# Performance work log

Measured on AMD Instinct MI355X. Metric: run time of the kernel, lower is better.

## Reference

```python
import jax, jax.numpy as jnp
import numpy as np

DIM = 1024
H = 16
HD = DIM // H
HIDDEN = 4096
EPS = 1e-5


def layer_norm(x, w, b):
    mu = jnp.mean(x, axis=-1, keepdims=True)
    var = jnp.mean(jnp.square(x - mu), axis=-1, keepdims=True)
    return (x - mu) * jax.lax.rsqrt(var + EPS) * w + b


def setup_inputs() -> dict:
    key = jax.random.key(0)
    ks = jax.random.split(key, 12)
    B, N = 4, 1024
    s = 0.02
    return {
        "x": jax.random.normal(ks[0], (B, N, DIM), jnp.float32),
        "rel_pos_bias": jax.random.normal(ks[1], (H, N, N), jnp.float32) * 0.1,
        "attn_mask": jax.random.randint(ks[2], (B, N), 0, 2, jnp.int32),
        "norm1_w": jnp.ones((DIM,), jnp.float32),
        "norm1_b": jnp.zeros((DIM,), jnp.float32),
        "qkv_w": jax.random.normal(ks[3], (3 * DIM, DIM), jnp.float32) * s,
        "q_bias": jnp.zeros((DIM,), jnp.float32),
        "v_bias": jnp.zeros((DIM,), jnp.float32),
        "proj_w": jax.random.normal(ks[4], (DIM, DIM), jnp.float32) * s,
        "proj_b": jnp.zeros((DIM,), jnp.float32),
        "norm2_w": jnp.ones((DIM,), jnp.float32),
        "norm2_b": jnp.zeros((DIM,), jnp.float32),
        "mlp_w1": jax.random.normal(ks[5], (HIDDEN, DIM), jnp.float32) * s,
        "mlp_b1": jnp.zeros((HIDDEN,), jnp.float32),
        "mlp_w2": jax.random.normal(ks[6], (DIM, HIDDEN), jnp.float32) * s,
        "mlp_b2": jnp.zeros((DIM,), jnp.float32),
    }


def attention(x, rel_pos_bias, attn_mask, qkv_w, q_bias, v_bias, proj_w, proj_b):
    B, N, C = x.shape
    scale = HD ** (-0.5)
    qkv_bias = jnp.concatenate([q_bias, jnp.zeros_like(v_bias), v_bias])
    qkv = x @ qkv_w.T + qkv_bias  # [B,N,3C]
    qkv = qkv.reshape(B, N, 3, H, HD).transpose(2, 0, 3, 1, 4)  # [3,B,H,N,hd]
    q, k, v = qkv[0] * scale, qkv[1], qkv[2]
    attn = jnp.einsum("bhqd,bhkd->bhqk", q, k) + rel_pos_bias[None]
    mask = attn_mask.astype(bool)[:, None, None, :]  # key padding mask
    attn = jnp.where(mask, attn, -jnp.inf)
    attn = jax.nn.softmax(attn, axis=-1)
    out = jnp.einsum("bhqk,bhkd->bhqd", attn, v)
    out = out.transpose(0, 2, 1, 3).reshape(B, N, C)
    return out @ proj_w.T + proj_b


def mlp(x, w1, b1, w2, b2):
    h = jax.nn.gelu(x @ w1.T + b1, approximate=False)
    return h @ w2.T + b2


def reference(x, rel_pos_bias, attn_mask, norm1_w, norm1_b, qkv_w, q_bias, v_bias,
              proj_w, proj_b, norm2_w, norm2_b, mlp_w1, mlp_b1, mlp_w2, mlp_b2):
    # pre-norm block, gamma=None, postnorm=False
    x = x + attention(layer_norm(x, norm1_w, norm1_b), rel_pos_bias, attn_mask,
                      qkv_w, q_bias, v_bias, proj_w, proj_b)
    x = x + mlp(layer_norm(x, norm2_w, norm2_b), mlp_w1, mlp_b1, mlp_w2, mlp_b2)
    return x
```

## Files before the change

### kernel.cpp

```cpp
#include <hip/hip_runtime.h>
#include <math.h>

#define DIM 1024
#define NHEAD 16
#define HD 64
#define HIDDEN 4096
#define SEQ 1024
#define BATCH 4
#define ROWS (BATCH*SEQ)

typedef __attribute__((ext_vector_type(8))) short bf16x8;
typedef __attribute__((ext_vector_type(4))) float f32x4;
typedef __attribute__((ext_vector_type(4))) unsigned short us4;

__device__ __forceinline__ unsigned short f2bf(float f) {
  unsigned u = __builtin_bit_cast(unsigned, f);
  u += 0x7fffu + ((u >> 16) & 1u);
  return (unsigned short)(u >> 16);
}

__device__ __forceinline__ float bf2f(unsigned short h) {
  unsigned u = (unsigned)h << 16;
  return __builtin_bit_cast(float, u);
}

__device__ __forceinline__ unsigned pkbf(float a, float b) {
  unsigned ua = __builtin_bit_cast(unsigned, a) + 0x8000u;
  unsigned ub = __builtin_bit_cast(unsigned, b) + 0x8000u;
  return __builtin_amdgcn_perm(ub, ua, 0x07060302u);
}

__device__ __forceinline__ float f3(float a, float b, float c) {
  return fmaxf(fmaxf(a, b), c);
}

__device__ __forceinline__ void glds16(const void* g, void* l) {
  __builtin_amdgcn_global_load_lds((const __attribute__((address_space(1))) void*)g,
                                   (__attribute__((address_space(3))) void*)l,
                                   16, 0, 0);
}

__global__ void cvt_all(const float* __restrict__ a, const float* __restrict__ b,
                        const float* __restrict__ c, const float* __restrict__ d,
                        unsigned short* __restrict__ oa, unsigned short* __restrict__ ob,
                        unsigned short* __restrict__ oc, unsigned short* __restrict__ od) {
  const int na = 3 * DIM * DIM / 4, nb = DIM * DIM / 4, nc = HIDDEN * DIM / 4, nd = DIM * HIDDEN / 4;
  const int total = na + nb + nc + nd;
  for (int i = blockIdx.x * blockDim.x + threadIdx.x; i < total; i += gridDim.x * blockDim.x) {
    const float* in; unsigned short* out; int j = i;
    if (j < na)             { in = a; out = oa; }
    else if ((j -= na) < nb){ in = b; out = ob; }
    else if ((j -= nb) < nc){ in = c; out = oc; }
    else                    { j -= nc; in = d; out = od; }
    float4 v = reinterpret_cast<const float4*>(in)[j];
    us4 o = { f2bf(v.x), f2bf(v.y), f2bf(v.z), f2bf(v.w) };
    reinterpret_cast<us4*>(out)[j] = o;
  }
}

template<bool IN_BF16>
__global__ void ln_kernel(const void* __restrict__ xv, const float* __restrict__ w,
                          const float* __restrict__ b, unsigned short* __restrict__ out) {
  int row = blockIdx.x;
  int t = threadIdx.x;
  float4 v;
  if (IN_BF16) {
    const unsigned short* xr = (const unsigned short*)xv + (size_t)row * DIM;
    us4 hv = *reinterpret_cast<const us4*>(xr + t * 4);
    v.x = bf2f(hv[0]); v.y = bf2f(hv[1]); v.z = bf2f(hv[2]); v.w = bf2f(hv[3]);
  } else {
    const float* xr = (const float*)xv + (size_t)row * DIM;
    v = *reinterpret_cast<const float4*>(xr + t * 4);
  }
  float s  = v.x + v.y + v.z + v.w;
  float s2 = v.x*v.x + v.y*v.y + v.z*v.z + v.w*v.w;
#pragma unroll
  for (int m = 1; m < 64; m <<= 1) { s += __shfl_xor(s, m); s2 += __shfl_xor(s2, m); }
  __shared__ float red[8];
  int wv = t >> 6, ln = t & 63;
  if (ln == 0) { red[wv] = s; red[4 + wv] = s2; }
  __syncthreads();
  s  = red[0] + red[1] + red[2] + red[3];
  s2 = red[4] + red[5] + red[6] + red[7];
  float mu  = s * (1.0f / DIM);
  float var = s2 * (1.0f / DIM) - mu * mu;
  float rs  = rsqrtf(var + 1e-5f);
  float4 wv4 = *reinterpret_cast<const float4*>(w + t * 4);
  float4 bv4 = *reinterpret_cast<const float4*>(b + t * 4);
  us4 o = { f2bf((v.x - mu) * rs * wv4.x + bv4.x),
            f2bf((v.y - mu) * rs * wv4.y + bv4.y),
            f2bf((v.z - mu) * rs * wv4.z + bv4.z),
            f2bf((v.w - mu) * rs * wv4.w + bv4.w) };
  *reinterpret_cast<us4*>(out + (size_t)row * DIM + t * 4) = o;
}

template<int MODE>
__global__ __launch_bounds__(256)
void gemm128k(const unsigned short* __restrict__ A, const unsigned short* __restrict__ Bw,
              int K, int N,
              const float* __restrict__ bias,
              unsigned short* __restrict__ outh)
{
  __shared__ unsigned short smA[2][128 * 64];
  __shared__ unsigned short smB[2][128 * 64];
  const int tid = threadIdx.x;
  const int wv = tid >> 6, ln = tid & 63;
  const int tile_m = blockIdx.x * 128, tile_n = blockIdx.y * 128;
  const int wm = (wv >> 1) * 64, wn = (wv & 1) * 64;

  const int srow8 = ln >> 3;
  const int sch8  = (ln & 7) ^ srow8;
  const unsigned short* gA = A  + (size_t)(tile_m + wv * 8 + srow8) * K + sch8 * 8;
  const unsigned short* gB = Bw + (size_t)(tile_n + wv * 8 + srow8) * K + sch8 * 8;

  f32x4 acc[4][4] = {};
  const int lr = ln & 15, g = ln >> 4;
  const int rx = lr & 7;

  auto stage = [&](int buf, int k0) {
#pragma unroll
    for (int p = 0; p < 4; p++)
      glds16(gA + (size_t)(p * 32) * K + k0, &smA[buf][(p * 32 + wv * 8) * 64]);
#pragma unroll
    for (int p = 0; p < 4; p++)
      glds16(gB + (size_t)(p * 32) * K + k0, &smB[buf][(p * 32 + wv * 8) * 64]);
  };

  stage(0, 0);
  __syncthreads();
  int cur = 0;
  for (int k0 = 0; k0 < K; k0 += 64) {
    if (k0 + 64 < K) stage(cur ^ 1, k0 + 64);
    bf16x8 af[4][2], bfr[4][2];
#pragma unroll
    for (int i = 0; i < 4; i++)
#pragma unroll
      for (int c = 0; c < 2; c++)
        af[i][c] = *reinterpret_cast<const bf16x8*>(
            &smA[cur][(wm + i * 16 + lr) * 64 + ((c * 4 + g) ^ rx) * 8]);
#pragma unroll
    for (int j = 0; j < 4; j++)
#pragma unroll
      for (int c = 0; c < 2; c++)
        bfr[j][c] = *reinterpret_cast<const bf16x8*>(
            &smB[cur][(wn + j * 16 + lr) * 64 + ((c * 4 + g) ^ rx) * 8]);
#pragma unroll
    for (int c = 0; c < 2; c++)
#pragma unroll
      for (int i = 0; i < 4; i++)
#pragma unroll
        for (int j = 0; j < 4; j++)
          acc[i][j] = __builtin_amdgcn_mfma_f32_16x16x32_bf16(af[i][c], bfr[j][c], acc[i][j], 0, 0, 0);
    __syncthreads();
    cur ^= 1;
  }

  const int lcol = ln & 15, lrow4 = (ln >> 4) * 4;
#pragma unroll
  for (int i = 0; i < 4; i++) {
#pragma unroll
    for (int j = 0; j < 4; j++) {
      int gm0 = tile_m + wm + i * 16 + lrow4;
      int gn  = tile_n + wn + j * 16 + lcol;
#pragma unroll
      for (int r = 0; r < 4; r++) {
        int gm = gm0 + r;
        float t2 = acc[i][j][r] + bias[gn];
        float u2 = 1.5957691216f * (t2 + 0.044715f * t2 * t2 * t2);
        float e  = __expf(u2);
        float th = 1.0f - 2.0f / (e + 1.0f);
        float gl = 0.5f * t2 * (1.0f + th);
        outh[(size_t)gm * N + gn] = f2bf(gl);
      }
    }
  }
}

template<int MODE>
__global__ __launch_bounds__(256)
void gemm64k(const unsigned short* __restrict__ A, const unsigned short* __restrict__ Bw,
             int K, int N,
             const float* __restrict__ bias, const void* __restrict__ resid,
             float* __restrict__ outf, unsigned short* __restrict__ outh,
             unsigned short* __restrict__ qo, unsigned short* __restrict__ ko,
             unsigned short* __restrict__ vto,
             const float* __restrict__ qbias, const float* __restrict__ vbias)
{
  __shared__ unsigned short smA[2][128 * 64];
  __shared__ unsigned short smB[2][64 * 64];
  const int tid = threadIdx.x;
  const int wv = tid >> 6, ln = tid & 63;
  const int tile_m = blockIdx.x * 128, tile_n = blockIdx.y * 64;
  const int wm = (wv >> 1) * 64, wn = (wv & 1) * 32;

  const int srow8 = ln >> 3;
  const int sch8  = (ln & 7) ^ srow8;
  const unsigned short* gA = A  + (size_t)(tile_m + wv * 8 + srow8) * K + sch8 * 8;
  const unsigned short* gB = Bw + (size_t)(tile_n + wv * 8 + srow8) * K + sch8 * 8;

  f32x4 acc[4][2] = {};
  const int lr = ln & 15, g = ln >> 4;
  const int rx = lr & 7;

  auto stage = [&](int buf, int k0) {
#pragma unroll
    for (int p = 0; p < 4; p++)
      glds16(gA + (size_t)(p * 32) * K + k0, &smA[buf][(p * 32 + wv * 8) * 64]);
#pragma unroll
    for (int p = 0; p < 2; p++)
      glds16(gB + (size_t)(p * 32) * K + k0, &smB[buf][(p * 32 + wv * 8) * 64]);
  };

  stage(0, 0);
  __syncthreads();
  int cur = 0;
  for (int k0 = 0; k0 < K; k0 += 64) {
    if (k0 + 64 < K) stage(cur ^ 1, k0 + 64);
    bf16x8 af[4][2], bfr[2][2];
#pragma unroll
    for (int i = 0; i < 4; i++)
#pragma unroll
      for (int c = 0; c < 2; c++)
        af[i][c] = *reinterpret_cast<const bf16x8*>(
            &smA[cur][(wm + i * 16 + lr) * 64 + ((c * 4 + g) ^ rx) * 8]);
#pragma unroll
    for (int j = 0; j < 2; j++)
#pragma unroll
      for (int c = 0; c < 2; c++)
        bfr[j][c] = *reinterpret_cast<const bf16x8*>(
            &smB[cur][(wn + j * 16 + lr) * 64 + ((c * 4 + g) ^ rx) * 8]);
#pragma unroll
    for (int c = 0; c < 2; c++)
#pragma unroll
      for (int i = 0; i < 4; i++)
#pragma unroll
        for (int j = 0; j < 2; j++)
          acc[i][j] = __builtin_amdgcn_mfma_f32_16x16x32_bf16(af[i][c], bfr[j][c], acc[i][j], 0, 0, 0);
    __syncthreads();
    cur ^= 1;
  }

  const int lcol = ln & 15, lrow4 = (ln >> 4) * 4;
#pragma unroll
  for (int i = 0; i < 4; i++) {
#pragma unroll
    for (int j = 0; j < 2; j++) {
      int gm0 = tile_m + wm + i * 16 + lrow4;
      int gn  = tile_n + wn + j * 16 + lcol;
#pragma unroll
      for (int r = 0; r < 4; r++) {
        int gm = gm0 + r;
        float val = acc[i][j][r];
        if (MODE == 0) {
          int b = gm >> 10, n = gm & 1023;
          if (gn < DIM) {
            float q = (val + qbias[gn]) * 0.125f;
            qo[(size_t)((b * NHEAD + (gn >> 6)) * SEQ + n) * HD + (gn & 63)] = f2bf(q);
          } else if (gn < 2 * DIM) {
            int g2 = gn - DIM;
            ko[(size_t)((b * NHEAD + (g2 >> 6)) * SEQ + n) * HD + (g2 & 63)] = f2bf(val);
          } else {
            int g3 = gn - 2 * DIM;
            vto[(size_t)((b * NHEAD + (g3 >> 6)) * HD + (g3 & 63)) * SEQ + n] = f2bf(val + vbias[g3]);
          }
        } else if (MODE == 1) {
          val += bias[gn] + ((const float*)resid)[(size_t)gm * N + gn];
          outh[(size_t)gm * N + gn] = f2bf(val);
        } else {
          val += bias[gn] + bf2f(((const unsigned short*)resid)[(size_t)gm * N + gn]);
          outf[(size_t)gm * N + gn] = val;
        }
      }
    }
  }
}

__global__ __launch_bounds__(512)
void attn_kernel(const unsigned short* __restrict__ qg, const unsigned short* __restrict__ kg,
                 const unsigned short* __restrict__ vtg, const float* __restrict__ rpb,
                 const int* __restrict__ amask, unsigned short* __restrict__ outh)
{
  constexpr int PSTR = 72;
  __shared__ unsigned short smK[2][64 * 64];
  __shared__ unsigned short smV[2][64 * 64];
  __shared__ unsigned short pls[8][16 * PSTR];
  const int tid = threadIdx.x;
  const int wv = tid >> 6, ln = tid & 63;
  const int bh = blockIdx.x, b = bh >> 4, h = bh & 15;
  const int q0 = blockIdx.y * 128 + wv * 16;
  const unsigned short* qb = qg  + (size_t)bh * SEQ * HD;
  const unsigned short* kb = kg  + (size_t)bh * SEQ * HD;
  const unsigned short* vb = vtg + (size_t)bh * HD * SEQ;
  const int* mp = amask + b * SEQ;
  unsigned short* myp = pls[wv];

  const int lcol = ln & 15, g = ln >> 4, lc8 = g * 8, lrow4 = g * 4;
  const int sw = (lcol & 7) << 3;
  const float* bprow = rpb + (size_t)h * SEQ * SEQ + (size_t)(q0 + lcol) * SEQ;

  const int srr = ln >> 3;
  const int scc = (ln & 7) ^ srr;

  bf16x8 aq0 = *reinterpret_cast<const bf16x8*>(qb + (size_t)(q0 + lcol) * HD + lc8);
  bf16x8 aq1 = *reinterpret_cast<const bf16x8*>(qb + (size_t)(q0 + lcol) * HD + 32 + lc8);

  f32x4 o[4] = {};
  float m = -1e30f, l = 0.f;

  auto stage = [&](int buf, int kt) {
    int row = wv * 8 + srr;
    glds16(kb + (size_t)(kt + row) * HD + scc * 8, &smK[buf][wv * 512]);
    glds16(vb + (size_t)row * SEQ + kt + scc * 8, &smV[buf][wv * 512]);
  };

  stage(0, 0);
  __syncthreads();

  for (int t = 0; t < SEQ / 64; t++) {
    const int cur = t & 1;
    const int kt = t * 64;
    float4 bv4[4]; int4 mv[4];
#pragma unroll
    for (int j = 0; j < 4; j++) {
      bv4[j] = *reinterpret_cast<const float4*>(bprow + kt + j * 16 + lrow4);
      mv[j]  = *reinterpret_cast<const int4*>(mp + kt + j * 16 + lrow4);
    }
    if (t < SEQ / 64 - 1) stage(cur ^ 1, kt + 64);

    f32x4 s[4];
    __builtin_amdgcn_s_setprio(1);
#pragma unroll
    for (int j = 0; j < 4; j++) {
      int r = j * 16 + lcol;
      bf16x8 bk0 = *reinterpret_cast<const bf16x8*>(&smK[cur][r * 64 + (lc8 ^ sw)]);
      bf16x8 bk1 = *reinterpret_cast<const bf16x8*>(&smK[cur][r * 64 + ((32 + lc8) ^ sw)]);
      f32x4 z = {0.f, 0.f, 0.f, 0.f};
      z = __builtin_amdgcn_mfma_f32_16x16x32_bf16(bk0, aq0, z, 0, 0, 0);
      z = __builtin_amdgcn_mfma_f32_16x16x32_bf16(bk1, aq1, z, 0, 0, 0);
      s[j] = z;
    }
    __builtin_amdgcn_s_setprio(0);
#pragma unroll
    for (int j = 0; j < 4; j++) {
      s[j][0] = mv[j].x ? s[j][0] + bv4[j].x : -1e30f;
      s[j][1] = mv[j].y ? s[j][1] + bv4[j].y : -1e30f;
      s[j][2] = mv[j].z ? s[j][2] + bv4[j].z : -1e30f;
      s[j][3] = mv[j].w ? s[j][3] + bv4[j].w : -1e30f;
    }
    float t0 = f3(s[0][0], s[0][1], s[0][2]);
    float t1 = f3(s[0][3], s[1][0], s[1][1]);
    float t2 = f3(s[1][2], s[1][3], s[2][0]);
    float t3 = f3(s[2][1], s[2][2], s[2][3]);
    float t4 = f3(s[3][0], s[3][1], s[3][2]);
    float pm = fmaxf(f3(t0, t1, t2), f3(t3, t4, s[3][3]));
    pm = fmaxf(pm, __shfl_xor(pm, 16));
    pm = fmaxf(pm, __shfl_xor(pm, 32));
    if (m < -1e29f || !__all(pm - m <= 8.0f)) {
      float mn = fmaxf(m, pm);
      float fr = __expf(m - mn);
      m = mn;
      l *= fr;
      float frq[4];
#pragma unroll
      for (int r = 0; r < 4; r++) frq[r] = __shfl(fr, lrow4 + r);
#pragma unroll
      for (int d = 0; d < 4; d++)
#pragma unroll
        for (int r = 0; r < 4; r++) o[d][r] *= frq[r];
    }
    float rs = 0.f;
#pragma unroll
    for (int j = 0; j < 4; j++)
#pragma unroll
      for (int r = 0; r < 4; r++) {
        float p = __expf(s[j][r] - m);
        s[j][r] = p;
        rs += p;
      }
    rs += __shfl_xor(rs, 16);
    rs += __shfl_xor(rs, 32);
    l += rs;
#pragma unroll
    for (int j = 0; j < 4; j++) {
      uint2 pw = { pkbf(s[j][0], s[j][1]), pkbf(s[j][2], s[j][3]) };
      *reinterpret_cast<uint2*>(myp + lcol * PSTR + j * 16 + lrow4) = pw;
    }
    asm volatile("s_waitcnt lgkmcnt(0)" ::: "memory");
    __builtin_amdgcn_sched_barrier(0);
    __builtin_amdgcn_s_setprio(1);
#pragma unroll
    for (int c = 0; c < 2; c++) {
      bf16x8 ap = *reinterpret_cast<const bf16x8*>(myp + lcol * PSTR + c * 32 + lc8);
#pragma unroll
      for (int d = 0; d < 4; d++) {
        int vr = d * 16 + lcol;
        bf16x8 bvv = *reinterpret_cast<const bf16x8*>(&smV[cur][vr * 64 + ((c * 32 + lc8) ^ sw)]);
        o[d] = __builtin_amdgcn_mfma_f32_16x16x32_bf16(ap, bvv, o[d], 0, 0, 0);
      }
    }
    __builtin_amdgcn_s_setprio(0);
    __syncthreads();
  }
  float linv = 1.0f / l;
  float lq[4];
#pragma unroll
  for (int r = 0; r < 4; r++) lq[r] = __shfl(linv, lrow4 + r);
#pragma unroll
  for (int d = 0; d < 4; d++)
#pragma unroll
    for (int r = 0; r < 4; r++)
      outh[(size_t)(b * SEQ + q0 + lrow4 + r) * DIM + h * HD + d * 16 + lcol] = f2bf(o[d][r] * lq[r]);
}

extern "C" void kernel_launch(void* const* d_in, const int* in_sizes, int n_in,
                              void* d_out, int out_size, void* d_ws, size_t ws_size,
                              hipStream_t stream)
{
  const float* x      = (const float*)d_in[0];
  const float* rpb    = (const float*)d_in[1];
  const int*   amask  = (const int*)d_in[2];
  const float* n1w    = (const float*)d_in[3];
  const float* n1b    = (const float*)d_in[4];
  const float* qkv_w  = (const float*)d_in[5];
  const float* q_bias = (const float*)d_in[6];
  const float* v_bias = (const float*)d_in[7];
  const float* proj_w = (const float*)d_in[8];
  const float* proj_b = (const float*)d_in[9];
  const float* n2w    = (const float*)d_in[10];
  const float* n2b    = (const float*)d_in[11];
  const float* w1     = (const float*)d_in[12];
  const float* b1     = (const float*)d_in[13];
  const float* w2     = (const float*)d_in[14];
  const float* b2     = (const float*)d_in[15];
  float* out = (float*)d_out;

  char* ws = (char*)d_ws;
  size_t off = 0;
  auto alloc = [&](size_t bytes) { char* p = ws + off; off += (bytes + 255) & ~(size_t)255; return p; };
  unsigned short* xn1    = (unsigned short*)alloc((size_t)ROWS * DIM * 2);
  unsigned short* xn2    = (unsigned short*)alloc((size_t)ROWS * DIM * 2);
  unsigned short* wqkv_h = (unsigned short*)alloc((size_t)3 * DIM * DIM * 2);
  unsigned short* wproj_h= (unsigned short*)alloc((size_t)DIM * DIM * 2);
  unsigned short* w1_h   = (unsigned short*)alloc((size_t)HIDDEN * DIM * 2);
  unsigned short* w2_h   = (unsigned short*)alloc((size_t)DIM * HIDDEN * 2);
  unsigned short* qh     = (unsigned short*)alloc((size_t)ROWS * DIM * 2);
  unsigned short* kh     = (unsigned short*)alloc((size_t)ROWS * DIM * 2);
  unsigned short* vth    = (unsigned short*)alloc((size_t)ROWS * DIM * 2);
  unsigned short* attn_h = (unsigned short*)alloc((size_t)ROWS * DIM * 2);
  unsigned short* xresh  = (unsigned short*)alloc((size_t)ROWS * DIM * 2);
  unsigned short* hmid   = (unsigned short*)alloc((size_t)ROWS * HIDDEN * 2);

  cvt_all<<<2048, 256, 0, stream>>>(qkv_w, proj_w, w1, w2, wqkv_h, wproj_h, w1_h, w2_h);

  ln_kernel<false><<<ROWS, 256, 0, stream>>>(x, n1w, n1b, xn1);
  gemm64k<0><<<dim3(ROWS / 128, 3 * DIM / 64), 256, 0, stream>>>(
      xn1, wqkv_h, DIM, 3 * DIM, nullptr, nullptr, nullptr, nullptr, qh, kh, vth, q_bias, v_bias);
  attn_kernel<<<dim3(BATCH * NHEAD, SEQ / 128), 512, 0, stream>>>(qh, kh, vth, rpb, amask, attn_h);
  gemm64k<1><<<dim3(ROWS / 128, DIM / 64), 256, 0, stream>>>(
      attn_h, wproj_h, DIM, DIM, proj_b, x, nullptr, xresh, nullptr, nullptr, nullptr, nullptr, nullptr);
  ln_kernel<true><<<ROWS, 256, 0, stream>>>(xresh, n2w, n2b, xn2);
  gemm128k<2><<<dim3(ROWS / 128, HIDDEN / 128), 256, 0, stream>>>(
      xn2, w1_h, DIM, HIDDEN, b1, hmid);
  gemm64k<3><<<dim3(ROWS / 128, DIM / 64), 256, 0, stream>>>(
      hmid, w2_h, HIDDEN, DIM, b2, xresh, out, nullptr, nullptr, nullptr, nullptr, nullptr, nullptr);
}
```

Baseline: 252.6 us.

## Overlap proj/MLP weight conversion with attention via extra blocks in attention grid

Splits the fp32-to-bf16 weight conversion: only the QKV weight is converted up front, and the proj/w1/w2 conversions move into 512 extra blocks appended to the attention kernel's grid. This takes the conversion of most weights off the critical path and lets it overlap with attention on idle CUs. The attention grid is flattened to 1D with bh and q-block indices recomputed. The converter blocks reserve the same LDS and 512-thread footprint as attention blocks, and they may compete with attention for bandwidth.

```diff
diff --git a/kernel.cpp b/kernel.cpp
--- a/kernel.cpp
+++ b/kernel.cpp
@@ -40,21 +40,12 @@
                                    16, 0, 0);
 }
 
-__global__ void cvt_all(const float* __restrict__ a, const float* __restrict__ b,
-                        const float* __restrict__ c, const float* __restrict__ d,
-                        unsigned short* __restrict__ oa, unsigned short* __restrict__ ob,
-                        unsigned short* __restrict__ oc, unsigned short* __restrict__ od) {
-  const int na = 3 * DIM * DIM / 4, nb = DIM * DIM / 4, nc = HIDDEN * DIM / 4, nd = DIM * HIDDEN / 4;
-  const int total = na + nb + nc + nd;
-  for (int i = blockIdx.x * blockDim.x + threadIdx.x; i < total; i += gridDim.x * blockDim.x) {
-    const float* in; unsigned short* out; int j = i;
-    if (j < na)             { in = a; out = oa; }
-    else if ((j -= na) < nb){ in = b; out = ob; }
-    else if ((j -= nb) < nc){ in = c; out = oc; }
-    else                    { j -= nc; in = d; out = od; }
-    float4 v = reinterpret_cast<const float4*>(in)[j];
+__global__ void cvt_qkv(const float* __restrict__ in, unsigned short* __restrict__ out) {
+  const int n4 = 3 * DIM * DIM / 4;
+  for (int i = blockIdx.x * blockDim.x + threadIdx.x; i < n4; i += gridDim.x * blockDim.x) {
+    float4 v = reinterpret_cast<const float4*>(in)[i];
     us4 o = { f2bf(v.x), f2bf(v.y), f2bf(v.z), f2bf(v.w) };
-    reinterpret_cast<us4*>(out)[j] = o;
+    reinterpret_cast<us4*>(out)[i] = o;
   }
 }
 
@@ -275,19 +266,42 @@
   }
 }
 
+#define NATT (BATCH * NHEAD * (SEQ / 128))
+#define NCVT 512
 __global__ __launch_bounds__(512)
 void attn_kernel(const unsigned short* __restrict__ qg, const unsigned short* __restrict__ kg,
                  const unsigned short* __restrict__ vtg, const float* __restrict__ rpb,
-                 const int* __restrict__ amask, unsigned short* __restrict__ outh)
+                 const int* __restrict__ amask, unsigned short* __restrict__ outh,
+                 const float* __restrict__ cpw, const float* __restrict__ cw1,
+                 const float* __restrict__ cw2,
+                 unsigned short* __restrict__ opw, unsigned short* __restrict__ ow1,
+                 unsigned short* __restrict__ ow2)
 {
   constexpr int PSTR = 72;
   __shared__ unsigned short smK[2][64 * 64];
   __shared__ unsigned short smV[2][64 * 64];
   __shared__ unsigned short pls[8][16 * PSTR];
+
+  if (blockIdx.x >= NATT) {
+    const int nb = DIM * DIM / 4, nc = HIDDEN * DIM / 4, nd = DIM * HIDDEN / 4;
+    const int total = nb + nc + nd;
+    for (int i = (blockIdx.x - NATT) * blockDim.x + threadIdx.x; i < total;
+         i += NCVT * blockDim.x) {
+      const float* in; unsigned short* out; int j = i;
+      if (j < nb)             { in = cpw; out = opw; }
+      else if ((j -= nb) < nc){ in = cw1; out = ow1; }
+      else                    { j -= nc; in = cw2; out = ow2; }
+      float4 v = reinterpret_cast<const float4*>(in)[j];
+      us4 o = { f2bf(v.x), f2bf(v.y), f2bf(v.z), f2bf(v.w) };
+      reinterpret_cast<us4*>(out)[j] = o;
+    }
+    return;
+  }
+
   const int tid = threadIdx.x;
   const int wv = tid >> 6, ln = tid & 63;
-  const int bh = blockIdx.x, b = bh >> 4, h = bh & 15;
-  const int q0 = blockIdx.y * 128 + wv * 16;
+  const int bh = blockIdx.x & 63, b = bh >> 4, h = bh & 15;
+  const int q0 = (blockIdx.x >> 6) * 128 + wv * 16;
   const unsigned short* qb = qg  + (size_t)bh * SEQ * HD;
   const unsigned short* kb = kg  + (size_t)bh * SEQ * HD;
   const unsigned short* vb = vtg + (size_t)bh * HD * SEQ;
@@ -450,12 +464,13 @@
   unsigned short* xresh  = (unsigned short*)alloc((size_t)ROWS * DIM * 2);
   unsigned short* hmid   = (unsigned short*)alloc((size_t)ROWS * HIDDEN * 2);
 
-  cvt_all<<<2048, 256, 0, stream>>>(qkv_w, proj_w, w1, w2, wqkv_h, wproj_h, w1_h, w2_h);
+  cvt_qkv<<<768, 256, 0, stream>>>(qkv_w, wqkv_h);
 
   ln_kernel<false><<<ROWS, 256, 0, stream>>>(x, n1w, n1b, xn1);
   gemm64k<0><<<dim3(ROWS / 128, 3 * DIM / 64), 256, 0, stream>>>(
       xn1, wqkv_h, DIM, 3 * DIM, nullptr, nullptr, nullptr, nullptr, qh, kh, vth, q_bias, v_bias);
-  attn_kernel<<<dim3(BATCH * NHEAD, SEQ / 128), 512, 0, stream>>>(qh, kh, vth, rpb, amask, attn_h);
+  attn_kernel<<<NATT + NCVT, 512, 0, stream>>>(qh, kh, vth, rpb, amask, attn_h,
+      proj_w, w1, w2, wproj_h, w1_h, w2_h);
   gemm64k<1><<<dim3(ROWS / 128, DIM / 64), 256, 0, stream>>>(
       attn_h, wproj_h, DIM, DIM, proj_b, x, nullptr, xresh, nullptr, nullptr, nullptr, nullptr, nullptr);
   ln_kernel<true><<<ROWS, 256, 0, stream>>>(xresh, n2w, n2b, xn2);
```

Measured after the change: 253.2 us. Within noise of the previous version (+0.2%).
